# Performance work log

Measured on AMD Instinct MI355X. Metric: run time of the kernel, lower is better.

The kernel has to match this reference:

```python
import jax, jax.numpy as jnp
import numpy as np

NEG = jnp.float32(-1e30)

def setup_inputs() -> dict:
    key = jax.random.key(0)
    k1, k2, k3, k4, k5, k6 = jax.random.split(key, 6)
    B, L, P, D = 16, 512, 32, 256
    inputs = jax.random.normal(k1, (B, L, D), dtype=jnp.float32)
    left_paths = jax.random.randint(k2, (B, L, P), 0, L)
    right_paths = jax.random.randint(k3, (B, L, P), 0, L)
    # path lengths >= 1 (a path always contains at least one node)
    left_lens = jax.random.randint(k4, (B, L), 1, P + 1)
    right_lens = jax.random.randint(k5, (B, L), 1, P + 1)
    sent_lens = jax.random.randint(k6, (B,), 1, L + 1)
    return {"inputs": inputs, "left_paths": left_paths, "right_paths": right_paths,
            "left_lens": left_lens, "right_lens": right_lens, "sent_lens": sent_lens}

def _path_max(inputs, paths, lens):
    # inputs: [B,L,D]; paths: [B,L,P]; lens: [B,L] -> masked max over path dim: [B,L,D]
    B = inputs.shape[0]
    P = paths.shape[-1]
    b_idx = jnp.arange(B)[:, None, None]
    gathered = inputs[b_idx, paths]                      # [B,L,P,D]
    mask = jnp.arange(P)[None, None, :] < lens[..., None]  # [B,L,P]
    return jnp.max(jnp.where(mask[..., None], gathered, NEG), axis=2)

def reference(inputs, left_paths, right_paths, left_lens, right_lens, sent_lens):
    L = inputs.shape[1]
    left_max = _path_max(inputs, left_paths, left_lens)    # [B,L,D]
    right_max = _path_max(inputs, right_paths, right_lens)  # [B,L,D]
    out = jnp.concatenate([left_max, right_max], axis=-1)   # [B,L,2D]
    token_mask = jnp.arange(L)[None, :] < sent_lens[:, None]  # zero-pad past sentence length
    return jnp.where(token_mask[..., None], out, 0.0)
```

## Files before the change

kernel.cpp:

```cpp
#include <hip/hip_runtime.h>


constexpr int BB = 16;
constexpr int LL = 512;
constexpr int PP = 32;
constexpr int D4 = 64;

typedef float v4f __attribute__((ext_vector_type(4)));

__device__ __forceinline__ v4f v4max(v4f a, v4f b) {
    v4f r;
    r.x = fmaxf(a.x, b.x);
    r.y = fmaxf(a.y, b.y);
    r.z = fmaxf(a.z, b.z);
    r.w = fmaxf(a.w, b.w);
    return r;
}

__global__ __launch_bounds__(64) void encoder_sdp_kernel(
    const v4f* __restrict__ inputs,
    const int* __restrict__ left_paths,
    const int* __restrict__ right_paths,
    const int* __restrict__ left_lens,
    const int* __restrict__ right_lens,
    const int* __restrict__ sent_lens,
    v4f*       __restrict__ out)
{
    const int blk  = blockIdx.x;
    const int side = blockIdx.y;
    const int b    = blk & (BB - 1);
    const int l    = blk >> 4;
    const int lane = threadIdx.x;
    const int bl   = b * LL + l;

    v4f* outp = out + (size_t)bl * (2 * D4) + side * D4 + lane;

    if (l >= sent_lens[b]) {
        v4f z = {0.f, 0.f, 0.f, 0.f};
        __builtin_nontemporal_store(z, outp);
        return;
    }

    const int* paths = side ? right_paths : left_paths;
    const int* lens  = side ? right_lens  : left_lens;
    const int  len   = lens[bl];
    const int* pbase = paths + (size_t)bl * PP;

    const v4f* base = inputs + (size_t)b * LL * D4 + lane;

    const float NEGV = -1e30f;
    v4f a0 = {NEGV, NEGV, NEGV, NEGV};
    v4f a1 = a0, a2 = a0, a3 = a0;

    const int lm1 = len - 1;
    const int nch = (len + 3) >> 2;
    for (int c = 0; c < nch; ++c) {
        const int p  = c << 2;
        const int i0 = pbase[p];
        const int i1 = pbase[min(p + 1, lm1)];
        const int i2 = pbase[min(p + 2, lm1)];
        const int i3 = pbase[min(p + 3, lm1)];
        const v4f v0 = base[(size_t)i0 * D4];
        const v4f v1 = base[(size_t)i1 * D4];
        const v4f v2 = base[(size_t)i2 * D4];
        const v4f v3 = base[(size_t)i3 * D4];
        a0 = v4max(a0, v0);
        a1 = v4max(a1, v1);
        a2 = v4max(a2, v2);
        a3 = v4max(a3, v3);
    }

    a0 = v4max(v4max(a0, a1), v4max(a2, a3));
    __builtin_nontemporal_store(a0, outp);
}

extern "C" void kernel_launch(void* const* d_in, const int* in_sizes, int n_in,
                              void* d_out, int out_size, void* d_ws, size_t ws_size,
                              hipStream_t stream) {
    const v4f* inputs      = (const v4f*)d_in[0];
    const int* left_paths  = (const int*)d_in[1];
    const int* right_paths = (const int*)d_in[2];
    const int* left_lens   = (const int*)d_in[3];
    const int* right_lens  = (const int*)d_in[4];
    const int* sent_lens   = (const int*)d_in[5];
    v4f*       out         = (v4f*)d_out;

    encoder_sdp_kernel<<<dim3(BB * LL, 2), 64, 0, stream>>>(
        inputs, left_paths, right_paths, left_lens, right_lens, sent_lens, out);
}
```

Before: 81.93 us.

## Pack four tokens per block and prefetch path indices with eight-wide gathers

```diff
diff --git a/kernel.cpp b/kernel.cpp
--- a/kernel.cpp
+++ b/kernel.cpp
@@ -5,6 +5,7 @@
 constexpr int LL = 512;
 constexpr int PP = 32;
 constexpr int D4 = 64;
+constexpr int CH = 8;
 
 typedef float v4f __attribute__((ext_vector_type(4)));
 
@@ -17,7 +18,7 @@
     return r;
 }
 
-__global__ __launch_bounds__(64) void encoder_sdp_kernel(
+__global__ __launch_bounds__(256, 6) void encoder_sdp_kernel(
     const v4f* __restrict__ inputs,
     const int* __restrict__ left_paths,
     const int* __restrict__ right_paths,
@@ -26,12 +27,12 @@
     const int* __restrict__ sent_lens,
     v4f*       __restrict__ out)
 {
-    const int blk  = blockIdx.x;
+    const int w    = threadIdx.x >> 6;
+    const int lane = threadIdx.x & 63;
+    const int b    = blockIdx.x & (BB - 1);
+    const int l    = ((blockIdx.x >> 4) << 2) + w;
     const int side = blockIdx.y;
-    const int b    = blk & (BB - 1);
-    const int l    = blk >> 4;
-    const int lane = threadIdx.x;
-    const int bl   = b * LL + l;
+    const int bl   = __builtin_amdgcn_readfirstlane(b * LL + l);
 
     v4f* outp = out + (size_t)bl * (2 * D4) + side * D4 + lane;
 
@@ -43,8 +44,15 @@
 
     const int* paths = side ? right_paths : left_paths;
     const int* lens  = side ? right_lens  : left_lens;
-    const int  len   = lens[bl];
     const int* pbase = paths + (size_t)bl * PP;
+
+    const int len = __builtin_amdgcn_readfirstlane(lens[bl]);
+    const int lm1 = len - 1;
+
+    int cur[CH];
+#pragma unroll
+    for (int k = 0; k < CH; ++k) cur[k] = pbase[k];
+    const int last = pbase[lm1];
 
     const v4f* base = inputs + (size_t)b * LL * D4 + lane;
 
@@ -52,22 +60,24 @@
     v4f a0 = {NEGV, NEGV, NEGV, NEGV};
     v4f a1 = a0, a2 = a0, a3 = a0;
 
-    const int lm1 = len - 1;
-    const int nch = (len + 3) >> 2;
+    const int nch = (len + CH - 1) / CH;
+    int p = 0;
     for (int c = 0; c < nch; ++c) {
-        const int p  = c << 2;
-        const int i0 = pbase[p];
-        const int i1 = pbase[min(p + 1, lm1)];
-        const int i2 = pbase[min(p + 2, lm1)];
-        const int i3 = pbase[min(p + 3, lm1)];
-        const v4f v0 = base[(size_t)i0 * D4];
-        const v4f v1 = base[(size_t)i1 * D4];
-        const v4f v2 = base[(size_t)i2 * D4];
-        const v4f v3 = base[(size_t)i3 * D4];
-        a0 = v4max(a0, v0);
-        a1 = v4max(a1, v1);
-        a2 = v4max(a2, v2);
-        a3 = v4max(a3, v3);
+        v4f v[CH];
+#pragma unroll
+        for (int k = 0; k < CH; ++k) {
+            const int j = (p + k <= lm1) ? cur[k] : last;
+            v[k] = base[(size_t)j * D4];
+        }
+#pragma unroll
+        for (int k = 0; k < CH; ++k) {
+            cur[k] = pbase[(p + CH + k) & (PP - 1)];
+        }
+        a0 = v4max(a0, v4max(v[0], v[4]));
+        a1 = v4max(a1, v4max(v[1], v[5]));
+        a2 = v4max(a2, v4max(v[2], v[6]));
+        a3 = v4max(a3, v4max(v[3], v[7]));
+        p += CH;
     }
 
     a0 = v4max(v4max(a0, a1), v4max(a2, a3));
@@ -85,6 +95,6 @@
     const int* sent_lens   = (const int*)d_in[5];
     v4f*       out         = (v4f*)d_out;
 
-    encoder_sdp_kernel<<<dim3(BB * LL, 2), 64, 0, stream>>>(
+    encoder_sdp_kernel<<<dim3(BB * (LL / 4), 2), 256, 0, stream>>>(
         inputs, left_paths, right_paths, left_lens, right_lens, sent_lens, out);
 }
```

Measured after the change: 81.59 us. No clear change (-0.4%).
